# Performance work log

Measured on AMD Instinct MI355X. Metric: run time of the kernel, lower is better.

The kernel has to match this reference:

```python
import jax, jax.numpy as jnp
import numpy as np

E = 512       # embed_dim
H = 8         # num_heads
DH = E // H   # head dim
F = 2048      # dim_feedforward
KS = 33       # NATTEN kernel_size (dilation=1)
NCLS = 1
B = 2
L = 4096      # local tokens (total seq = L + NCLS)
EPS = 1e-5


def layernorm(x, g, b):
    mu = jnp.mean(x, axis=-1, keepdims=True)
    var = jnp.mean(jnp.square(x - mu), axis=-1, keepdims=True)
    return (x - mu) * jax.lax.rsqrt(var + EPS) * g + b


def natten_1d(x, qkv_w, qkv_b, proj_w, proj_b):
    # Neighborhood attention 1D, dilation=1, non-causal, no rel-pos bias.
    b, l, e = x.shape
    qkv = x @ qkv_w.T + qkv_b                       # [b, l, 3E]
    q, k, v = jnp.split(qkv, 3, axis=-1)
    q = q.reshape(b, l, H, DH) * (DH ** -0.5)
    k = k.reshape(b, l, H, DH)
    v = v.reshape(b, l, H, DH)
    # NATTEN window: centered, shifted at edges to keep exactly KS in-bounds neighbors
    starts = jnp.clip(jnp.arange(l) - KS // 2, 0, l - KS)   # [l]
    idx = starts[:, None] + jnp.arange(KS)                  # [l, KS]
    kn = k[:, idx]                                          # [b, l, KS, H, DH]
    vn = v[:, idx]                                          # [b, l, KS, H, DH]
    attn = jnp.einsum('blhd,blkhd->bhlk', q, kn)
    attn = jax.nn.softmax(attn, axis=-1)
    out = jnp.einsum('bhlk,blkhd->blhd', attn, vn).reshape(b, l, e)
    return out @ proj_w.T + proj_b


def global_mha(q_in, kv_in, in_w, in_b, out_w, out_b):
    # torch nn.MultiheadAttention, batch_first, no masks
    bq, lq, e = q_in.shape
    lk = kv_in.shape[1]
    wq, wk, wv = jnp.split(in_w, 3, axis=0)
    bqp, bkp, bvp = jnp.split(in_b, 3, axis=0)
    q = (q_in @ wq.T + bqp).reshape(bq, lq, H, DH) * (DH ** -0.5)
    k = (kv_in @ wk.T + bkp).reshape(bq, lk, H, DH)
    v = (kv_in @ wv.T + bvp).reshape(bq, lk, H, DH)
    attn = jax.nn.softmax(jnp.einsum('bqhd,bkhd->bhqk', q, k), axis=-1)
    out = jnp.einsum('bhqk,bkhd->bqhd', attn, v).reshape(bq, lq, e)
    return out @ out_w.T + out_b


def setup_inputs() -> dict:
    key = jax.random.key(0)
    ks = jax.random.split(key, 16)
    s = 0.02
    return {
        'x': jax.random.normal(ks[0], (B, L + NCLS, E), jnp.float32),
        'ln1_g': jnp.ones((E,), jnp.float32),
        'ln1_b': jnp.zeros((E,), jnp.float32),
        'qkv_w': jax.random.normal(ks[1], (3 * E, E), jnp.float32) * s,
        'qkv_b': jnp.zeros((3 * E,), jnp.float32),
        'na_proj_w': jax.random.normal(ks[2], (E, E), jnp.float32) * s,
        'na_proj_b': jnp.zeros((E,), jnp.float32),
        'in_proj_w': jax.random.normal(ks[3], (3 * E, E), jnp.float32) * s,
        'in_proj_b': jnp.zeros((3 * E,), jnp.float32),
        'out_w': jax.random.normal(ks[4], (E, E), jnp.float32) * s,
        'out_b': jnp.zeros((E,), jnp.float32),
        'ln2_g': jnp.ones((E,), jnp.float32),
        'ln2_b': jnp.zeros((E,), jnp.float32),
        'fc1_w': jax.random.normal(ks[5], (F, E), jnp.float32) * s,
        'fc1_b': jnp.zeros((F,), jnp.float32),
        'fc2_w': jax.random.normal(ks[6], (E, F), jnp.float32) * s,
        'fc2_b': jnp.zeros((E,), jnp.float32),
    }


def reference(x, ln1_g, ln1_b, qkv_w, qkv_b, na_proj_w, na_proj_b,
              in_proj_w, in_proj_b, out_w, out_b, ln2_g, ln2_b,
              fc1_w, fc1_b, fc2_w, fc2_b):
    res = x
    xn = layernorm(x, ln1_g, ln1_b)
    x_local = natten_1d(xn[:, :-NCLS, :], qkv_w, qkv_b, na_proj_w, na_proj_b)
    tmp_key = jnp.concatenate([x_local, xn[:, -NCLS:, :]], axis=1)
    x_cls = global_mha(xn[:, -NCLS:, :], tmp_key, in_proj_w, in_proj_b, out_w, out_b)
    x = res + jnp.concatenate([x_local, x_cls], axis=1)
    res = x
    xn = layernorm(x, ln2_g, ln2_b)
    h = jax.nn.silu(xn @ fc1_w.T + fc1_b)
    return res + (h @ fc2_w.T + fc2_b)
```

## Files before the change

kernel.cpp:

```cpp
#include <hip/hip_runtime.h>
#include <hip/hip_bf16.h>
#include <cstdint>
#include <cstddef>

#define E    512
#define H    8
#define DHD  64
#define FDIM 2048
#define KS   33
#define BB   2
#define LL   4096
#define LP1  4097
#define NTOK 8194
#define NLOC 8192

typedef unsigned short ushort_t;
typedef __bf16 bf16x8_t __attribute__((ext_vector_type(8)));
typedef float  f32x4_t  __attribute__((ext_vector_type(4)));

__device__ __forceinline__ float b2f(unsigned short h) {
  union { unsigned int u; float f; } un; un.u = ((unsigned int)h) << 16; return un.f;
}
__device__ __forceinline__ unsigned short f2b(float f) {
  union { float f; unsigned int u; } un; un.f = f;
  unsigned int u = un.u;
  return (unsigned short)((u + 0x7FFFu + ((u >> 16) & 1u)) >> 16);
}

__device__ __forceinline__ void gload16(const ushort_t* g, ushort_t* l) {
  __builtin_amdgcn_global_load_lds(
      (const __attribute__((address_space(1))) void*)g,
      (__attribute__((address_space(3))) void*)l,
      16, 0, 0);
}

__device__ __forceinline__ int xcd_remap(int hw, int n) {
  int xcd = hw & 7, j = hw >> 3;
  int q = n >> 3, r = n & 7;
  return (xcd < r ? xcd * (q + 1) : r * (q + 1) + (xcd - r) * q) + j;
}

#define BM 128

template<int BNT, int ACT, int OUTF, int ADDRES, int INRM, int OUTRM, int PARTIAL>
__global__ __launch_bounds__(256) void gemm_bt(
    const ushort_t* __restrict__ A, const ushort_t* __restrict__ W,
    const float* __restrict__ bias, float* __restrict__ outF,
    ushort_t* __restrict__ outB, const float* __restrict__ res,
    int M, int N, int K, int klen, int ny, int nz)
{
  constexpr int NFRAG = BNT / 32;
  __shared__ ushort_t Alds[2][BM * 64];
  __shared__ ushort_t Blds[2][BNT * 64];
  const int t    = threadIdx.x;
  const int lane = t & 63;
  const int w    = t >> 6;
  const int wr   = w >> 1, wc = w & 1;

  const int Lid = xcd_remap(blockIdx.x, gridDim.x);
  const int bx  = Lid / (ny * nz);
  const int rem = Lid % (ny * nz);
  const int z   = rem / ny;
  const int by  = rem % ny;
  const int bmBase = bx * BM;
  const int bnBase = by * BNT;
  const int kbeg = z * klen;

  f32x4_t zero = {0.f, 0.f, 0.f, 0.f};
  f32x4_t acc[4][NFRAG];
  #pragma unroll
  for (int m = 0; m < 4; ++m)
    #pragma unroll
    for (int n = 0; n < NFRAG; ++n) acc[m][n] = zero;

  const int srow = t >> 3;
  const int jsw8 = ((t & 7) ^ (srow & 7)) * 8;
  int arow[4];
  #pragma unroll
  for (int r = 0; r < 4; ++r) {
    int rr = bmBase + r * 32 + srow;
    if (INRM) rr += rr >> 12;
    else if (rr >= M) rr = M - 1;
    arow[r] = rr;
  }
  int brow[NFRAG];
  #pragma unroll
  for (int r = 0; r < NFRAG; ++r) brow[r] = bnBase + r * 32 + srow;

  const int frow = lane & 15;
  const int g    = lane >> 4;

  auto STAGE = [&](int s, int k0) {
    #pragma unroll
    for (int r = 0; r < 4; ++r)
      gload16(A + (size_t)arow[r] * K + k0 + jsw8, &Alds[s][(size_t)(r * 256 + t) * 8]);
    #pragma unroll
    for (int r = 0; r < NFRAG; ++r)
      gload16(W + (size_t)brow[r] * K + k0 + jsw8, &Blds[s][(size_t)(r * 256 + t) * 8]);
  };

  const int nt = klen >> 6;
  STAGE(0, kbeg);

  for (int it = 0; it < nt; ++it) {
    const int cur = it & 1;
    asm volatile("s_waitcnt vmcnt(0)" ::: "memory");
    __builtin_amdgcn_s_barrier();
    __builtin_amdgcn_sched_barrier(0);
    if (it + 1 < nt) STAGE(cur ^ 1, kbeg + (it + 1) * 64);
    bf16x8_t af[2][4], bfv[2][NFRAG];
    #pragma unroll
    for (int kk2 = 0; kk2 < 2; ++kk2) {
      const int kosw = ((kk2 * 4 + g) ^ (frow & 7)) << 4;
      #pragma unroll
      for (int m = 0; m < 4; ++m) {
        int row = wr * 64 + m * 16 + frow;
        af[kk2][m] = *reinterpret_cast<const bf16x8_t*>((char*)Alds[cur] + row * 128 + kosw);
      }
      #pragma unroll
      for (int n = 0; n < NFRAG; ++n) {
        int row = wc * (BNT / 2) + n * 16 + frow;
        bfv[kk2][n] = *reinterpret_cast<const bf16x8_t*>((char*)Blds[cur] + row * 128 + kosw);
      }
    }
    #pragma unroll
    for (int kk2 = 0; kk2 < 2; ++kk2)
      #pragma unroll
      for (int m = 0; m < 4; ++m)
        #pragma unroll
        for (int n = 0; n < NFRAG; ++n)
          acc[m][n] = __builtin_amdgcn_mfma_f32_16x16x32_bf16(af[kk2][m], bfv[kk2][n], acc[m][n], 0, 0, 0);
  }

  const int rbase = g * 4;
  const int cbase = frow;
  float* po = nullptr;
  if (PARTIAL) po = (z == 0) ? outF : (float*)outB;
  #pragma unroll
  for (int m = 0; m < 4; ++m) {
    #pragma unroll
    for (int r = 0; r < 4; ++r) {
      int gr = bmBase + wr * 64 + m * 16 + rbase + r;
      if (gr < M) {
        int orow = OUTRM ? gr + (gr >> 12) : gr;
        #pragma unroll
        for (int n = 0; n < NFRAG; ++n) {
          int gc = bnBase + wc * (BNT / 2) + n * 16 + cbase;
          float v = acc[m][n][r];
          if (PARTIAL) {
            po[(size_t)orow * N + gc] = v;
          } else {
            v += bias[gc];
            if (ACT == 1) v = v / (1.f + __expf(-v));
            if (ADDRES) v += res[(size_t)gr * N + gc];
            if (OUTF) outF[(size_t)orow * N + gc] = v;
            else      outB[(size_t)orow * N + gc] = f2b(v);
          }
        }
      }
    }
  }
}

__global__ __launch_bounds__(256) void fc2_reduce(
    float* __restrict__ out, const float* __restrict__ p0,
    const float* __restrict__ bias, const float* __restrict__ xa)
{
  size_t i = (size_t)blockIdx.x * 256 + threadIdx.x;
  float4 o = reinterpret_cast<const float4*>(out)[i];
  float4 a = reinterpret_cast<const float4*>(p0)[i];
  float4 x = reinterpret_cast<const float4*>(xa)[i];
  float4 bcol = reinterpret_cast<const float4*>(bias)[i & 127];
  o.x += a.x + x.x + bcol.x;
  o.y += a.y + x.y + bcol.y;
  o.z += a.z + x.z + bcol.z;
  o.w += a.w + x.w + bcol.w;
  reinterpret_cast<float4*>(out)[i] = o;
}

__global__ __launch_bounds__(256) void ln_fused1(
    const float* __restrict__ x, const float* __restrict__ g,
    const float* __restrict__ be, ushort_t* __restrict__ xn,
    ushort_t* __restrict__ tmpk)
{
  __shared__ float sh[4];
  const int row = blockIdx.x;
  const int t = threadIdx.x;
  const float* xr = x + (size_t)row * E;
  float v0 = xr[t], v1 = xr[t + 256];
  float sum = v0 + v1;
  #pragma unroll
  for (int o = 32; o; o >>= 1) sum += __shfl_xor(sum, o);
  if ((t & 63) == 0) sh[t >> 6] = sum;
  __syncthreads();
  float mean = (sh[0] + sh[1] + sh[2] + sh[3]) * (1.f / E);
  __syncthreads();
  float d0 = v0 - mean, d1 = v1 - mean;
  float vs = d0 * d0 + d1 * d1;
  #pragma unroll
  for (int o = 32; o; o >>= 1) vs += __shfl_xor(vs, o);
  if ((t & 63) == 0) sh[t >> 6] = vs;
  __syncthreads();
  float var = (sh[0] + sh[1] + sh[2] + sh[3]) * (1.f / E);
  float rstd = rsqrtf(var + 1e-5f);
  unsigned short o0 = f2b(d0 * rstd * g[t] + be[t]);
  unsigned short o1 = f2b(d1 * rstd * g[t + 256] + be[t + 256]);
  xn[(size_t)row * E + t] = o0;
  xn[(size_t)row * E + t + 256] = o1;
  if ((row % LP1) == LL) {
    tmpk[(size_t)row * E + t] = o0;
    tmpk[(size_t)row * E + t + 256] = o1;
  }
}

__global__ __launch_bounds__(256) void resid_ln2(
    const float* __restrict__ x, const ushort_t* __restrict__ tmpk,
    const float* __restrict__ xcls, const float* __restrict__ g,
    const float* __restrict__ be, float* __restrict__ xa,
    ushort_t* __restrict__ xn2)
{
  __shared__ float sh[4];
  const int row = blockIdx.x;
  const int b = row / LP1, l = row % LP1;
  const int t = threadIdx.x;
  float a0, a1;
  if (l < LL) { a0 = b2f(tmpk[(size_t)row * E + t]); a1 = b2f(tmpk[(size_t)row * E + t + 256]); }
  else        { a0 = xcls[b * E + t];                a1 = xcls[b * E + t + 256]; }
  float v0 = x[(size_t)row * E + t] + a0;
  float v1 = x[(size_t)row * E + t + 256] + a1;
  xa[(size_t)row * E + t] = v0;
  xa[(size_t)row * E + t + 256] = v1;
  float sum = v0 + v1;
  #pragma unroll
  for (int o = 32; o; o >>= 1) sum += __shfl_xor(sum, o);
  if ((t & 63) == 0) sh[t >> 6] = sum;
  __syncthreads();
  float mean = (sh[0] + sh[1] + sh[2] + sh[3]) * (1.f / E);
  __syncthreads();
  float d0 = v0 - mean, d1 = v1 - mean;
  float vs = d0 * d0 + d1 * d1;
  #pragma unroll
  for (int o = 32; o; o >>= 1) vs += __shfl_xor(vs, o);
  if ((t & 63) == 0) sh[t >> 6] = vs;
  __syncthreads();
  float var = (sh[0] + sh[1] + sh[2] + sh[3]) * (1.f / E);
  float rstd = rsqrtf(var + 1e-5f);
  xn2[(size_t)row * E + t]       = f2b(d0 * rstd * g[t] + be[t]);
  xn2[(size_t)row * E + t + 256] = f2b(d1 * rstd * g[t + 256] + be[t + 256]);
}

__global__ __launch_bounds__(256) void natten_mfma(
    const ushort_t* __restrict__ qkv, ushort_t* __restrict__ out)
{
  __shared__ ushort_t KP[4][64 * 64];
  __shared__ ushort_t VT[4][64 * 72];
  const int w    = threadIdx.x >> 6;
  const int lane = threadIdx.x & 63;
  const int task = blockIdx.x * 4 + w;
  const int h  = task & 7;
  const int qb = (task >> 3) & 127;
  const int b  = task >> 10;
  const int l0 = qb * 32;
  const int kb = l0 - 16;
  const ushort_t* base = qkv + (size_t)b * LL * (3 * E);
  ushort_t* Klds = KP[w];
  ushort_t* Vt   = VT[w];

  {
    const int rsub = lane >> 3;
    const int d0   = (lane & 7) * 8;
    #pragma unroll
    for (int i = 0; i < 8; ++i) {
      int row = i * 8 + rsub;
      int gl = kb + row; gl = gl < 0 ? 0 : (gl > LL - 1 ? LL - 1 : gl);
      bf16x8_t kv = *reinterpret_cast<const bf16x8_t*>(
          base + (size_t)gl * (3 * E) + E + h * 64 + d0);
      int ba = (row * 128 + d0 * 2) ^ ((row & 7) << 4);
      *reinterpret_cast<bf16x8_t*>((char*)Klds + ba) = kv;
    }
  }
  {
    const int a  = lane & 7;
    const int c8 = lane >> 3;
    unsigned int* Vt32 = (unsigned int*)Vt;
    #pragma unroll
    for (int i = 0; i < 4; ++i) {
      int rp = i * 8 + c8;
      int g0 = kb + rp * 2;     g0 = g0 < 0 ? 0 : (g0 > LL - 1 ? LL - 1 : g0);
      int g1 = kb + rp * 2 + 1; g1 = g1 < 0 ? 0 : (g1 > LL - 1 ? LL - 1 : g1);
      const ushort_t* v0 = base + (size_t)g0 * (3 * E) + 2 * E + h * 64 + a * 8;
      const ushort_t* v1 = base + (size_t)g1 * (3 * E) + 2 * E + h * 64 + a * 8;
      ushort4 x0 = *(const ushort4*)v0,       x1 = *(const ushort4*)v1;
      ushort4 y0 = *(const ushort4*)(v0 + 4), y1 = *(const ushort4*)(v1 + 4);
      int d = a * 8;
      Vt32[(d + 0) * 36 + rp] = (unsigned)x0.x | ((unsigned)x1.x << 16);
      Vt32[(d + 1) * 36 + rp] = (unsigned)x0.y | ((unsigned)x1.y << 16);
      Vt32[(d + 2) * 36 + rp] = (unsigned)x0.z | ((unsigned)x1.z << 16);
      Vt32[(d + 3) * 36 + rp] = (unsigned)x0.w | ((unsigned)x1.w << 16);
      Vt32[(d + 4) * 36 + rp] = (unsigned)y0.x | ((unsigned)y1.x << 16);
      Vt32[(d + 5) * 36 + rp] = (unsigned)y0.y | ((unsigned)y1.y << 16);
      Vt32[(d + 6) * 36 + rp] = (unsigned)y0.z | ((unsigned)y1.z << 16);
      Vt32[(d + 7) * 36 + rp] = (unsigned)y0.w | ((unsigned)y1.w << 16);
    }
  }

  const int p = lane & 15, g = lane >> 4;
  bf16x8_t qf[2][2];
  #pragma unroll
  for (int mt = 0; mt < 2; ++mt)
    #pragma unroll
    for (int ks = 0; ks < 2; ++ks)
      qf[mt][ks] = *reinterpret_cast<const bf16x8_t*>(
          base + (size_t)(l0 + mt * 16 + p) * (3 * E) + h * 64 + ks * 32 + g * 8);

  f32x4_t zero = {0.f, 0.f, 0.f, 0.f};
  f32x4_t accS[2][4];
  #pragma unroll
  for (int mt = 0; mt < 2; ++mt)
    #pragma unroll
    for (int nt = 0; nt < 4; ++nt) accS[mt][nt] = zero;
  #pragma unroll
  for (int ks = 0; ks < 2; ++ks) {
    bf16x8_t kf[4];
    #pragma unroll
    for (int nt = 0; nt < 4; ++nt) {
      int row = nt * 16 + p;
      int ba = (row * 128 + (ks * 32 + g * 8) * 2) ^ ((row & 7) << 4);
      kf[nt] = *reinterpret_cast<const bf16x8_t*>((char*)Klds + ba);
    }
    #pragma unroll
    for (int mt = 0; mt < 2; ++mt)
      #pragma unroll
      for (int nt = 0; nt < 4; ++nt)
        accS[mt][nt] = __builtin_amdgcn_mfma_f32_16x16x32_bf16(qf[mt][ks], kf[nt], accS[mt][nt], 0, 0, 0);
  }

  ushort_t* Plds = Klds;
  #pragma unroll
  for (int mt = 0; mt < 2; ++mt) {
    #pragma unroll
    for (int r = 0; r < 4; ++r) {
      int lq = l0 + mt * 16 + g * 4 + r;
      int st = lq - 16; st = st < 0 ? 0 : (st > LL - KS ? LL - KS : st);
      int clo = st - kb, chi = clo + 32;
      float sv[4];
      float mx = -1e30f;
      #pragma unroll
      for (int nt = 0; nt < 4; ++nt) {
        int c = nt * 16 + p;
        float s = accS[mt][nt][r] * 0.125f;
        s = (c >= clo && c <= chi) ? s : -1e30f;
        sv[nt] = s;
        mx = fmaxf(mx, s);
      }
      mx = fmaxf(mx, __shfl_xor(mx, 1));
      mx = fmaxf(mx, __shfl_xor(mx, 2));
      mx = fmaxf(mx, __shfl_xor(mx, 4));
      mx = fmaxf(mx, __shfl_xor(mx, 8));
      float sum = 0.f;
      #pragma unroll
      for (int nt = 0; nt < 4; ++nt) { float e = __expf(sv[nt] - mx); sv[nt] = e; sum += e; }
      sum += __shfl_xor(sum, 1);
      sum += __shfl_xor(sum, 2);
      sum += __shfl_xor(sum, 4);
      sum += __shfl_xor(sum, 8);
      float inv = 1.f / sum;
      int q = mt * 16 + g * 4 + r;
      #pragma unroll
      for (int nt = 0; nt < 4; ++nt)
        Plds[q * 72 + nt * 16 + p] = f2b(sv[nt] * inv);
    }
  }

  f32x4_t accO[2][4];
  #pragma unroll
  for (int mt = 0; mt < 2; ++mt)
    #pragma unroll
    for (int nt = 0; nt < 4; ++nt) accO[mt][nt] = zero;
  #pragma unroll
  for (int ks = 0; ks < 2; ++ks) {
    bf16x8_t pf[2], vf[4];
    #pragma unroll
    for (int mt = 0; mt < 2; ++mt)
      pf[mt] = *reinterpret_cast<const bf16x8_t*>(
          (char*)Plds + (mt * 16 + p) * 144 + (ks * 32 + g * 8) * 2);
    #pragma unroll
    for (int nt = 0; nt < 4; ++nt)
      vf[nt] = *reinterpret_cast<const bf16x8_t*>(
          (char*)Vt + (nt * 16 + p) * 144 + (ks * 32 + g * 8) * 2);
    #pragma unroll
    for (int mt = 0; mt < 2; ++mt)
      #pragma unroll
      for (int nt = 0; nt < 4; ++nt)
        accO[mt][nt] = __builtin_amdgcn_mfma_f32_16x16x32_bf16(pf[mt], vf[nt], accO[mt][nt], 0, 0, 0);
  }

  #pragma unroll
  for (int mt = 0; mt < 2; ++mt) {
    #pragma unroll
    for (int r = 0; r < 4; ++r) {
      int lq = l0 + mt * 16 + g * 4 + r;
      ushort_t* orow = out + ((size_t)(b * LL) + lq) * E + h * 64;
      #pragma unroll
      for (int nt = 0; nt < 4; ++nt)
        orow[nt * 16 + p] = f2b(accO[mt][nt][r]);
    }
  }
}

__global__ __launch_bounds__(256) void qcls_kernel(
    const ushort_t* __restrict__ xn, const float* __restrict__ inw,
    const float* __restrict__ inb, float* __restrict__ qcls)
{
  int i = blockIdx.x * 256 + threadIdx.x;
  int b = i >> 9, d = i & 511;
  const ushort_t* xr = xn + ((size_t)b * LP1 + LL) * E;
  const float* wr = inw + (size_t)d * E;
  float s = 0.f;
  for (int e = 0; e < E; e += 4) {
    ushort4 xv = *reinterpret_cast<const ushort4*>(xr + e);
    s += b2f(xv.x) * wr[e] + b2f(xv.y) * wr[e + 1] + b2f(xv.z) * wr[e + 2] + b2f(xv.w) * wr[e + 3];
  }
  qcls[i] = (s + inb[d]) * 0.125f;
}

__global__ __launch_bounds__(256) void gscore_kernel(
    const float* __restrict__ qcls, const ushort_t* __restrict__ kv,
    float* __restrict__ sc)
{
  const int wav = blockIdx.x * 4 + (threadIdx.x >> 6);
  if (wav >= BB * LP1) return;
  const int lane = threadIdx.x & 63;
  const int b = wav / LP1, j = wav % LP1;
  const ushort_t* kr = kv + (size_t)wav * 1024 + lane * 8;
  const float* q = qcls + b * E + lane * 8;
  ushort4 ka = *reinterpret_cast<const ushort4*>(kr);
  ushort4 kb4 = *reinterpret_cast<const ushort4*>(kr + 4);
  float s = b2f(ka.x) * q[0] + b2f(ka.y) * q[1] + b2f(ka.z) * q[2] + b2f(ka.w) * q[3]
          + b2f(kb4.x) * q[4] + b2f(kb4.y) * q[5] + b2f(kb4.z) * q[6] + b2f(kb4.w) * q[7];
  s += __shfl_xor(s, 1); s += __shfl_xor(s, 2); s += __shfl_xor(s, 4);
  if ((lane & 7) == 0) sc[((size_t)(b * 8) + (lane >> 3)) * LP1 + j] = s;
}

__global__ __launch_bounds__(256) void gsoftmax_kernel(float* __restrict__ sc)
{
  float* row = sc + (size_t)blockIdx.x * LP1;
  __shared__ float sh[4];
  const int t = threadIdx.x;
  float m = -1e30f;
  for (int i = t; i < LP1; i += 256) m = fmaxf(m, row[i]);
  #pragma unroll
  for (int o = 32; o; o >>= 1) m = fmaxf(m, __shfl_xor(m, o));
  if ((t & 63) == 0) sh[t >> 6] = m;
  __syncthreads();
  m = fmaxf(fmaxf(sh[0], sh[1]), fmaxf(sh[2], sh[3]));
  __syncthreads();
  float s = 0.f;
  for (int i = t; i < LP1; i += 256) { float e = __expf(row[i] - m); row[i] = e; s += e; }
  #pragma unroll
  for (int o = 32; o; o >>= 1) s += __shfl_xor(s, o);
  if ((t & 63) == 0) sh[t >> 6] = s;
  __syncthreads();
  float inv = 1.f / (sh[0] + sh[1] + sh[2] + sh[3]);
  for (int i = t; i < LP1; i += 256) row[i] *= inv;
}

__global__ __launch_bounds__(256) void gpv_kernel(
    const float* __restrict__ sc, const ushort_t* __restrict__ kv,
    float* __restrict__ parts)
{
  __shared__ float red[4][64];
  const int bh = blockIdx.y;
  const int b = bh >> 3, h = bh & 7;
  const int c = blockIdx.x;
  const int lane = threadIdx.x & 63, s4 = threadIdx.x >> 6;
  const int j0 = c * 512;
  const int jend = (j0 + 512 < LP1) ? j0 + 512 : LP1;
  const float* prow = sc + (size_t)bh * LP1;
  const ushort_t* vbase = kv + (size_t)b * LP1 * 1024 + 512 + h * 64 + lane;
  float acc = 0.f;
  for (int j = j0 + s4; j < jend; j += 4)
    acc += prow[j] * b2f(vbase[(size_t)j * 1024]);
  red[s4][lane] = acc;
  __syncthreads();
  if (s4 == 0)
    parts[((size_t)c * 16 + bh) * 64 + lane] = red[0][lane] + red[1][lane] + red[2][lane] + red[3][lane];
}

__global__ void gpv_reduce(const float* __restrict__ parts, float* __restrict__ oc)
{
  int i = blockIdx.x * 256 + threadIdx.x;
  if (i < BB * E) {
    float s = 0.f;
    #pragma unroll
    for (int c = 0; c < 9; ++c) s += parts[c * 1024 + i];
    oc[i] = s;
  }
}

__global__ __launch_bounds__(256) void xcls_kernel(
    const float* __restrict__ oc, const float* __restrict__ ow,
    const float* __restrict__ ob, float* __restrict__ xc)
{
  int i = blockIdx.x * 256 + threadIdx.x;
  if (i >= BB * E) return;
  int b = i >> 9, n = i & 511;
  const float* o = oc + b * E;
  const float* wr = ow + (size_t)n * E;
  float s = ob[n];
  for (int m = 0; m < E; ++m) s += o[m] * wr[m];
  xc[i] = s;
}

__global__ void cvt_all(
    const float* __restrict__ s0, ushort_t* __restrict__ d0, int n0,
    const float* __restrict__ s1, ushort_t* __restrict__ d1, int n1,
    const float* __restrict__ s2, ushort_t* __restrict__ d2, int n2,
    const float* __restrict__ s3, ushort_t* __restrict__ d3, int n3,
    const float* __restrict__ s4, ushort_t* __restrict__ d4, int n4)
{
  int i = (blockIdx.x * 256 + threadIdx.x) * 4;
  const float* s; ushort_t* d;
  if (i < n0)                { s = s0; d = d0; }
  else if ((i -= n0) < n1)   { s = s1; d = d1; }
  else if ((i -= n1) < n2)   { s = s2; d = d2; }
  else if ((i -= n2) < n3)   { s = s3; d = d3; }
  else if ((i -= n3) < n4)   { s = s4; d = d4; }
  else return;
  float4 v = *reinterpret_cast<const float4*>(s + i);
  ushort4 o;
  o.x = f2b(v.x); o.y = f2b(v.y); o.z = f2b(v.z); o.w = f2b(v.w);
  *reinterpret_cast<ushort4*>(d + i) = o;
}

extern "C" void kernel_launch(void* const* d_in, const int* in_sizes, int n_in,
                              void* d_out, int out_size, void* d_ws, size_t ws_size,
                              hipStream_t stream)
{
  const float* x      = (const float*)d_in[0];
  const float* ln1_g  = (const float*)d_in[1];
  const float* ln1_b  = (const float*)d_in[2];
  const float* qkv_w  = (const float*)d_in[3];
  const float* qkv_b  = (const float*)d_in[4];
  const float* na_w   = (const float*)d_in[5];
  const float* na_b   = (const float*)d_in[6];
  const float* in_w   = (const float*)d_in[7];
  const float* in_b   = (const float*)d_in[8];
  const float* out_w  = (const float*)d_in[9];
  const float* out_b  = (const float*)d_in[10];
  const float* ln2_g  = (const float*)d_in[11];
  const float* ln2_b  = (const float*)d_in[12];
  const float* fc1_w  = (const float*)d_in[13];
  const float* fc1_b  = (const float*)d_in[14];
  const float* fc2_w  = (const float*)d_in[15];
  const float* fc2_b  = (const float*)d_in[16];
  float* out = (float*)d_out;

  char* pws = (char*)d_ws;
  size_t off = 0;
  auto alloc = [&](size_t bytes) {
    void* r = pws + off; off = (off + bytes + 255) & ~(size_t)255; return r;
  };
  ushort_t* w_qkv = (ushort_t*)alloc((size_t)3 * E * E * 2);
  ushort_t* w_na  = (ushort_t*)alloc((size_t)E * E * 2);
  ushort_t* w_in  = (ushort_t*)alloc((size_t)3 * E * E * 2);
  ushort_t* w_fc1 = (ushort_t*)alloc((size_t)FDIM * E * 2);
  ushort_t* w_fc2 = (ushort_t*)alloc((size_t)E * FDIM * 2);
  ushort_t* xn1   = (ushort_t*)alloc((size_t)NTOK * E * 2);
  char*     bigR  = (char*)alloc((size_t)NTOK * FDIM * 2);
  ushort_t* qkvb  = (ushort_t*)bigR;
  ushort_t* natt  = (ushort_t*)(bigR + (size_t)NLOC * 3 * E * 2);
  ushort_t* kvg   = (ushort_t*)bigR;
  ushort_t* hbuf  = (ushort_t*)bigR;
  ushort_t* tmpk  = (ushort_t*)alloc((size_t)NTOK * E * 2);
  float*    sc    = (float*)alloc((size_t)BB * H * LP1 * 4);
  float*    qcls  = (float*)alloc(1024 * 4);
  float*    parts = (float*)alloc(9 * 16 * 64 * 4);
  float*    oc    = (float*)alloc(1024 * 4);
  float*    xcls  = (float*)alloc(1024 * 4);
  float*    xa    = (float*)alloc((size_t)NTOK * E * 4);
  ushort_t* xn2   = xn1;
  size_t off_before_s0 = off;
  float*    s0    = (float*)alloc((size_t)NTOK * E * 4);
  const bool can_split = (off <= ws_size);
  if (!can_split) off = off_before_s0;

  cvt_all<<<3840, 256, 0, stream>>>(
      qkv_w, w_qkv, 3 * E * E,
      na_w,  w_na,  E * E,
      in_w,  w_in,  3 * E * E,
      fc1_w, w_fc1, FDIM * E,
      fc2_w, w_fc2, E * FDIM);

  ln_fused1<<<NTOK, 256, 0, stream>>>(x, ln1_g, ln1_b, xn1, tmpk);
  qcls_kernel<<<4, 256, 0, stream>>>(xn1, in_w, in_b, qcls);
  gemm_bt<128,0,0,0,1,0,0><<<64 * 12, 256, 0, stream>>>(
      xn1, w_qkv, qkv_b, nullptr, qkvb, nullptr, NLOC, 3 * E, E, E, 12, 1);
  natten_mfma<<<512, 256, 0, stream>>>(qkvb, natt);
  gemm_bt<128,0,0,0,0,1,0><<<64 * 4, 256, 0, stream>>>(
      natt, w_na, na_b, nullptr, tmpk, nullptr, NLOC, E, E, E, 4, 1);
  gemm_bt<128,0,0,0,0,0,0><<<65 * 8, 256, 0, stream>>>(
      tmpk, w_in + (size_t)E * E, in_b + E, nullptr, kvg, nullptr, NTOK, 1024, E, E, 8, 1);
  gscore_kernel<<<(BB * LP1 + 3) / 4, 256, 0, stream>>>(qcls, kvg, sc);
  gsoftmax_kernel<<<BB * H, 256, 0, stream>>>(sc);
  gpv_kernel<<<dim3(9, BB * H), 256, 0, stream>>>(sc, kvg, parts);
  gpv_reduce<<<4, 256, 0, stream>>>(parts, oc);
  xcls_kernel<<<4, 256, 0, stream>>>(oc, out_w, out_b, xcls);
  resid_ln2<<<NTOK, 256, 0, stream>>>(x, tmpk, xcls, ln2_g, ln2_b, xa, xn2);
  gemm_bt<128,1,0,0,0,0,0><<<65 * 16, 256, 0, stream>>>(
      xn2, w_fc1, fc1_b, nullptr, hbuf, nullptr, NTOK, FDIM, E, E, 16, 1);
  if (can_split) {
    gemm_bt<128,0,0,0,0,0,1><<<65 * 4 * 2, 256, 0, stream>>>(
        hbuf, w_fc2, fc2_b, s0, (ushort_t*)out, nullptr, NTOK, E, FDIM, FDIM / 2, 4, 2);
    fc2_reduce<<<(NTOK * E / 4) / 256, 256, 0, stream>>>(out, s0, fc2_b, xa);
  } else {
    gemm_bt<128,0,1,1,0,0,0><<<65 * 4, 256, 0, stream>>>(
        hbuf, w_fc2, fc2_b, out, nullptr, xa, NTOK, E, FDIM, FDIM, 4, 1);
  }
}
```

Before: 282.0 us.

## Generalize GEMM tiling to 256-row tiles with 512-thread blocks and MFMA priority

Templates the bf16 MFMA GEMM on block M/N tile size, thread count and warp-column layout. The QKV, KV-projection, FC1 and FC2 GEMMs move to 256x256 or 256x128 tiles with 512 threads (8 waves), which raises data reuse per LDS stage and cuts the block count. It also interleaves fragment loads with MFMAs per k-substep and raises wave priority around the MFMA bursts. The trade-off is more LDS per block, higher register pressure, fewer blocks for the 256-CU device, and larger edge waste on the 8194-row GEMMs.

```diff
diff --git a/kernel.cpp b/kernel.cpp
--- a/kernel.cpp
+++ b/kernel.cpp
@@ -40,63 +40,66 @@
   return (xcd < r ? xcd * (q + 1) : r * (q + 1) + (xcd - r) * q) + j;
 }
 
-#define BM 128
-
-template<int BNT, int ACT, int OUTF, int ADDRES, int INRM, int OUTRM, int PARTIAL>
-__global__ __launch_bounds__(256) void gemm_bt(
+template<int BMT, int BNT, int NTH, int WC, int ACT, int OUTF, int ADDRES,
+         int INRM, int OUTRM, int PARTIAL>
+__global__ __launch_bounds__(NTH) void gemm_bt(
     const ushort_t* __restrict__ A, const ushort_t* __restrict__ W,
     const float* __restrict__ bias, float* __restrict__ outF,
     ushort_t* __restrict__ outB, const float* __restrict__ res,
     int M, int N, int K, int klen, int ny, int nz)
 {
-  constexpr int NFRAG = BNT / 32;
-  __shared__ ushort_t Alds[2][BM * 64];
+  constexpr int MF  = BMT / 32;
+  constexpr int NF  = BNT / (WC * 16);
+  constexpr int AR  = (BMT * 64) / (8 * NTH);
+  constexpr int BR  = (BNT * 64) / (8 * NTH);
+  constexpr int RPR = NTH / 8;
+  __shared__ ushort_t Alds[2][BMT * 64];
   __shared__ ushort_t Blds[2][BNT * 64];
   const int t    = threadIdx.x;
   const int lane = t & 63;
   const int w    = t >> 6;
-  const int wr   = w >> 1, wc = w & 1;
+  const int wr   = w / WC, wc = w % WC;
 
   const int Lid = xcd_remap(blockIdx.x, gridDim.x);
   const int bx  = Lid / (ny * nz);
   const int rem = Lid % (ny * nz);
   const int z   = rem / ny;
   const int by  = rem % ny;
-  const int bmBase = bx * BM;
+  const int bmBase = bx * BMT;
   const int bnBase = by * BNT;
   const int kbeg = z * klen;
 
   f32x4_t zero = {0.f, 0.f, 0.f, 0.f};
-  f32x4_t acc[4][NFRAG];
-  #pragma unroll
-  for (int m = 0; m < 4; ++m)
-    #pragma unroll
-    for (int n = 0; n < NFRAG; ++n) acc[m][n] = zero;
+  f32x4_t acc[MF][NF];
+  #pragma unroll
+  for (int m = 0; m < MF; ++m)
+    #pragma unroll
+    for (int n = 0; n < NF; ++n) acc[m][n] = zero;
 
   const int srow = t >> 3;
   const int jsw8 = ((t & 7) ^ (srow & 7)) * 8;
-  int arow[4];
-  #pragma unroll
-  for (int r = 0; r < 4; ++r) {
-    int rr = bmBase + r * 32 + srow;
+  int arow[AR];
+  #pragma unroll
+  for (int r = 0; r < AR; ++r) {
+    int rr = bmBase + r * RPR + srow;
     if (INRM) rr += rr >> 12;
     else if (rr >= M) rr = M - 1;
     arow[r] = rr;
   }
-  int brow[NFRAG];
-  #pragma unroll
-  for (int r = 0; r < NFRAG; ++r) brow[r] = bnBase + r * 32 + srow;
+  int brow[BR];
+  #pragma unroll
+  for (int r = 0; r < BR; ++r) brow[r] = bnBase + r * RPR + srow;
 
   const int frow = lane & 15;
   const int g    = lane >> 4;
 
   auto STAGE = [&](int s, int k0) {
     #pragma unroll
-    for (int r = 0; r < 4; ++r)
-      gload16(A + (size_t)arow[r] * K + k0 + jsw8, &Alds[s][(size_t)(r * 256 + t) * 8]);
-    #pragma unroll
-    for (int r = 0; r < NFRAG; ++r)
-      gload16(W + (size_t)brow[r] * K + k0 + jsw8, &Blds[s][(size_t)(r * 256 + t) * 8]);
+    for (int r = 0; r < AR; ++r)
+      gload16(A + (size_t)arow[r] * K + k0 + jsw8, &Alds[s][(size_t)(r * NTH + t) * 8]);
+    #pragma unroll
+    for (int r = 0; r < BR; ++r)
+      gload16(W + (size_t)brow[r] * K + k0 + jsw8, &Blds[s][(size_t)(r * NTH + t) * 8]);
   };
 
   const int nt = klen >> 6;
@@ -108,28 +111,28 @@
     __builtin_amdgcn_s_barrier();
     __builtin_amdgcn_sched_barrier(0);
     if (it + 1 < nt) STAGE(cur ^ 1, kbeg + (it + 1) * 64);
-    bf16x8_t af[2][4], bfv[2][NFRAG];
     #pragma unroll
     for (int kk2 = 0; kk2 < 2; ++kk2) {
+      bf16x8_t af[MF], bfv[NF];
       const int kosw = ((kk2 * 4 + g) ^ (frow & 7)) << 4;
       #pragma unroll
-      for (int m = 0; m < 4; ++m) {
-        int row = wr * 64 + m * 16 + frow;
-        af[kk2][m] = *reinterpret_cast<const bf16x8_t*>((char*)Alds[cur] + row * 128 + kosw);
+      for (int m = 0; m < MF; ++m) {
+        int row = wr * (BMT / 2) + m * 16 + frow;
+        af[m] = *reinterpret_cast<const bf16x8_t*>((char*)Alds[cur] + row * 128 + kosw);
       }
       #pragma unroll
-      for (int n = 0; n < NFRAG; ++n) {
-        int row = wc * (BNT / 2) + n * 16 + frow;
-        bfv[kk2][n] = *reinterpret_cast<const bf16x8_t*>((char*)Blds[cur] + row * 128 + kosw);
+      for (int n = 0; n < NF; ++n) {
+        int row = wc * (BNT / WC) + n * 16 + frow;
+        bfv[n] = *reinterpret_cast<const bf16x8_t*>((char*)Blds[cur] + row * 128 + kosw);
       }
+      __builtin_amdgcn_s_setprio(1);
+      #pragma unroll
+      for (int m = 0; m < MF; ++m)
+        #pragma unroll
+        for (int n = 0; n < NF; ++n)
+          acc[m][n] = __builtin_amdgcn_mfma_f32_16x16x32_bf16(af[m], bfv[n], acc[m][n], 0, 0, 0);
+      __builtin_amdgcn_s_setprio(0);
     }
-    #pragma unroll
-    for (int kk2 = 0; kk2 < 2; ++kk2)
-      #pragma unroll
-      for (int m = 0; m < 4; ++m)
-        #pragma unroll
-        for (int n = 0; n < NFRAG; ++n)
-          acc[m][n] = __builtin_amdgcn_mfma_f32_16x16x32_bf16(af[kk2][m], bfv[kk2][n], acc[m][n], 0, 0, 0);
   }
 
   const int rbase = g * 4;
@@ -137,15 +140,15 @@
   float* po = nullptr;
   if (PARTIAL) po = (z == 0) ? outF : (float*)outB;
   #pragma unroll
-  for (int m = 0; m < 4; ++m) {
+  for (int m = 0; m < MF; ++m) {
     #pragma unroll
     for (int r = 0; r < 4; ++r) {
-      int gr = bmBase + wr * 64 + m * 16 + rbase + r;
+      int gr = bmBase + wr * (BMT / 2) + m * 16 + rbase + r;
       if (gr < M) {
         int orow = OUTRM ? gr + (gr >> 12) : gr;
         #pragma unroll
-        for (int n = 0; n < NFRAG; ++n) {
-          int gc = bnBase + wc * (BNT / 2) + n * 16 + cbase;
+        for (int n = 0; n < NF; ++n) {
+          int gc = bnBase + wc * (BNT / WC) + n * 16 + cbase;
           float v = acc[m][n][r];
           if (PARTIAL) {
             po[(size_t)orow * N + gc] = v;
@@ -594,12 +597,12 @@
 
   ln_fused1<<<NTOK, 256, 0, stream>>>(x, ln1_g, ln1_b, xn1, tmpk);
   qcls_kernel<<<4, 256, 0, stream>>>(xn1, in_w, in_b, qcls);
-  gemm_bt<128,0,0,0,1,0,0><<<64 * 12, 256, 0, stream>>>(
-      xn1, w_qkv, qkv_b, nullptr, qkvb, nullptr, NLOC, 3 * E, E, E, 12, 1);
+  gemm_bt<256,256,512,4, 0,0,0,1,0,0><<<32 * 6, 512, 0, stream>>>(
+      xn1, w_qkv, qkv_b, nullptr, qkvb, nullptr, NLOC, 3 * E, E, E, 6, 1);
   natten_mfma<<<512, 256, 0, stream>>>(qkvb, natt);
-  gemm_bt<128,0,0,0,0,1,0><<<64 * 4, 256, 0, stream>>>(
+  gemm_bt<128,128,256,2, 0,0,0,0,1,0><<<64 * 4, 256, 0, stream>>>(
       natt, w_na, na_b, nullptr, tmpk, nullptr, NLOC, E, E, E, 4, 1);
-  gemm_bt<128,0,0,0,0,0,0><<<65 * 8, 256, 0, stream>>>(
+  gemm_bt<256,128,512,4, 0,0,0,0,0,0><<<33 * 8, 512, 0, stream>>>(
       tmpk, w_in + (size_t)E * E, in_b + E, nullptr, kvg, nullptr, NTOK, 1024, E, E, 8, 1);
   gscore_kernel<<<(BB * LP1 + 3) / 4, 256, 0, stream>>>(qcls, kvg, sc);
   gsoftmax_kernel<<<BB * H, 256, 0, stream>>>(sc);
@@ -607,14 +610,14 @@
   gpv_reduce<<<4, 256, 0, stream>>>(parts, oc);
   xcls_kernel<<<4, 256, 0, stream>>>(oc, out_w, out_b, xcls);
   resid_ln2<<<NTOK, 256, 0, stream>>>(x, tmpk, xcls, ln2_g, ln2_b, xa, xn2);
-  gemm_bt<128,1,0,0,0,0,0><<<65 * 16, 256, 0, stream>>>(
-      xn2, w_fc1, fc1_b, nullptr, hbuf, nullptr, NTOK, FDIM, E, E, 16, 1);
+  gemm_bt<256,256,512,4, 1,0,0,0,0,0><<<33 * 8, 512, 0, stream>>>(
+      xn2, w_fc1, fc1_b, nullptr, hbuf, nullptr, NTOK, FDIM, E, E, 8, 1);
   if (can_split) {
-    gemm_bt<128,0,0,0,0,0,1><<<65 * 4 * 2, 256, 0, stream>>>(
+    gemm_bt<256,128,512,4, 0,0,0,0,0,1><<<33 * 4 * 2, 512, 0, stream>>>(
         hbuf, w_fc2, fc2_b, s0, (ushort_t*)out, nullptr, NTOK, E, FDIM, FDIM / 2, 4, 2);
     fc2_reduce<<<(NTOK * E / 4) / 256, 256, 0, stream>>>(out, s0, fc2_b, xa);
   } else {
-    gemm_bt<128,0,1,1,0,0,0><<<65 * 4, 256, 0, stream>>>(
+    gemm_bt<256,128,512,4, 0,0,1,1,0,0><<<33 * 4, 512, 0, stream>>>(
         hbuf, w_fc2, fc2_b, out, nullptr, xa, NTOK, E, FDIM, FDIM, 4, 1);
   }
 }
```

After: 317.7 us. 1.13x slower.
